# Kernel tuning notes

Measured on AMD Instinct MI355X. Metric: run time of the kernel, lower is better.

The kernel has to match this reference:

```python
import jax, jax.numpy as jnp
import numpy as np

SIGMA = 8.0
C_SIZE = 512
STRIDE = 8
BG_RATIO = 0.15
EPS = 1e-5


def setup_inputs() -> dict:
    key = jax.random.key(0)
    k1, k2 = jax.random.split(key)
    B, N = 16, 512
    # head-point coordinates uniformly in the crop [0, C_SIZE)
    points = jax.random.uniform(k1, (B, N, 2), dtype=jnp.float32) * C_SIZE
    # per-image shortest side sizes, realistic crop scales
    st_sizes = jax.random.uniform(k2, (B,), dtype=jnp.float32) * 256.0 + 256.0
    return {"points": points, "st_sizes": st_sizes}


def reference(points, st_sizes):
    # pixel-center coordinates of the downsampled density grid, [C]
    cood = jnp.arange(0, C_SIZE, STRIDE, dtype=jnp.float32) + STRIDE / 2.0
    B, N, _ = points.shape
    C = cood.shape[0]
    x = points[..., 0]  # [B, N]
    y = points[..., 1]  # [B, N]
    # (x - c)^2 == -2*x*c + x^2 + c^2 (the matmul trick in the original)
    x_dis = (x[..., None] - cood) ** 2  # [B, N, C]
    y_dis = (y[..., None] - cood) ** 2  # [B, N, C]
    # dis[b, p, i, j] = (y_p - cood_i)^2 + (x_p - cood_j)^2
    dis = y_dis[:, :, :, None] + x_dis[:, :, None, :]  # [B, N, C, C]
    dis = dis.reshape(B, N, C * C)  # [B, N, M]
    # background distance: per-pixel min over points, clamped at 0
    min_dis = jnp.clip(jnp.min(dis, axis=1, keepdims=True), 0.0)  # [B, 1, M]
    bg_dis = (st_sizes[:, None, None] * BG_RATIO) ** 2 / (min_dis + EPS)
    dis = jnp.concatenate([dis, bg_dis], axis=1)  # [B, N+1, M]
    logits = -dis / (2.0 * SIGMA ** 2)
    # softmax over the point (+background) axis, per pixel
    return jax.nn.softmax(logits, axis=1)
```

## Files before the change

### kernel.cpp

```cpp
#include <hip/hip_runtime.h>
#include <hip/hip_bf16.h>
#include <cstddef>

constexpr int NPT = 512;
constexpr int C   = 64;
constexpr int M   = C * C;
constexpr int NP1 = NPT + 1;
constexpr float K = 1.0f / 128.0f;
constexpr float BG_RATIO = 0.15f;
constexpr float EPS = 1e-5f;

__global__ __launch_bounds__(256) void pp_kernel(
    const float* __restrict__ points,
    const float* __restrict__ st,
    float* __restrict__ out)
{
    const int b    = blockIdx.x >> 6;
    const int i    = blockIdx.x & 63;
    const int t    = threadIdx.x;
    const int lane = t & 63;
    const int w    = t >> 6;
    const int jg   = t & 15;
    const int pc   = t >> 4;

    const float cy  = (float)(i * 8 + 4);
    const float cx0 = (float)(jg * 32 + 4);
    const float cx1 = cx0 + 8.0f;
    const float cx2 = cx0 + 16.0f;
    const float cx3 = cx0 + 24.0f;

    __shared__ float2 pts[NPT];
    __shared__ float4 redmin[4][16];
    __shared__ float4 redsum[4][16];
    __shared__ float  rs[C];
    __shared__ float  bgs[C];

    const float2* pb = (const float2*)(points + (size_t)b * NPT * 2);
    for (int p = t; p < NPT; p += 256) pts[p] = pb[p];
    __syncthreads();

    const int p0 = pc * 32;

    float4 mn = make_float4(3.4e38f, 3.4e38f, 3.4e38f, 3.4e38f);
    float4 sm = make_float4(0.f, 0.f, 0.f, 0.f);
    #pragma unroll 4
    for (int k = 0; k < 32; ++k) {
        float2 xy = pts[p0 + k];
        float dy  = xy.y - cy;
        float dy2 = dy * dy;
        float dx0 = xy.x - cx0, dx1 = xy.x - cx1, dx2 = xy.x - cx2, dx3 = xy.x - cx3;
        float d0 = fmaf(dx0, dx0, dy2);
        float d1 = fmaf(dx1, dx1, dy2);
        float d2 = fmaf(dx2, dx2, dy2);
        float d3 = fmaf(dx3, dx3, dy2);
        mn.x = fminf(mn.x, d0); mn.y = fminf(mn.y, d1);
        mn.z = fminf(mn.z, d2); mn.w = fminf(mn.w, d3);
        sm.x += __expf(-d0 * K); sm.y += __expf(-d1 * K);
        sm.z += __expf(-d2 * K); sm.w += __expf(-d3 * K);
    }

    #pragma unroll
    for (int off = 16; off <= 32; off <<= 1) {
        mn.x = fminf(mn.x, __shfl_xor(mn.x, off));
        mn.y = fminf(mn.y, __shfl_xor(mn.y, off));
        mn.z = fminf(mn.z, __shfl_xor(mn.z, off));
        mn.w = fminf(mn.w, __shfl_xor(mn.w, off));
        sm.x += __shfl_xor(sm.x, off);
        sm.y += __shfl_xor(sm.y, off);
        sm.z += __shfl_xor(sm.z, off);
        sm.w += __shfl_xor(sm.w, off);
    }
    if (lane < 16) { redmin[w][lane] = mn; redsum[w][lane] = sm; }
    __syncthreads();

    if (t < C) {
        const float* rm = (const float*)redmin;
        const float* rq = (const float*)redsum;
        float m0 = fminf(fminf(rm[t], rm[64 + t]), fminf(rm[128 + t], rm[192 + t]));
        float s0 = (rq[t] + rq[64 + t]) + (rq[128 + t] + rq[192 + t]);
        float ss = st[b] * BG_RATIO;
        float bg = (ss * ss) / (m0 + EPS);
        float tot = s0 + __expf(-bg * K);
        bgs[t] = bg;
        rs[t]  = 1.0f / tot;
    }
    __syncthreads();

    const float4 r4 = *(const float4*)&rs[jg * 4];

    float* ob = out + (size_t)b * NP1 * M + (size_t)p0 * M + i * C + jg * 4;
    #pragma unroll 4
    for (int k = 0; k < 32; ++k) {
        float2 xy = pts[p0 + k];
        float dy  = xy.y - cy;
        float dy2 = dy * dy;
        float dx0 = xy.x - cx0, dx1 = xy.x - cx1, dx2 = xy.x - cx2, dx3 = xy.x - cx3;
        float4 v;
        v.x = __expf(-fmaf(dx0, dx0, dy2) * K) * r4.x;
        v.y = __expf(-fmaf(dx1, dx1, dy2) * K) * r4.y;
        v.z = __expf(-fmaf(dx2, dx2, dy2) * K) * r4.z;
        v.w = __expf(-fmaf(dx3, dx3, dy2) * K) * r4.w;
        *(float4*)(ob + (size_t)k * M) = v;
    }

    if (t < C) {
        out[(size_t)b * NP1 * M + (size_t)NPT * M + i * C + t] =
            __expf(-bgs[t] * K) * rs[t];
    }
}

extern "C" void kernel_launch(void* const* d_in, const int* in_sizes, int n_in,
                              void* d_out, int out_size, void* d_ws, size_t ws_size,
                              hipStream_t stream) {
    const float* points = (const float*)d_in[0];
    const float* st     = (const float*)d_in[1];
    float* out          = (float*)d_out;

    const int B = in_sizes[1];
    dim3 grid(B * C);
    dim3 block(256);
    pp_kernel<<<grid, block, 0, stream>>>(points, st, out);
}
```

Before: 141.1 us.

## Split into denominator and row-contiguous store kernels via workspace

The fused kernel is split in two. The first kernel computes the per-pixel softmax reciprocal and the background channel, and writes the reciprocal to workspace. The second kernel launches one block per (batch, point) and writes each full output row of M floats contiguously, instead of scattered 256-byte chunks across many rows. The exponentials also switch to exp2f with a prescaled constant. The trade-off is an extra launch, a workspace round trip, and recomputing the point loads in the second kernel.

```diff
diff --git a/kernel.cpp b/kernel.cpp
--- a/kernel.cpp
+++ b/kernel.cpp
@@ -6,14 +6,15 @@
 constexpr int C   = 64;
 constexpr int M   = C * C;
 constexpr int NP1 = NPT + 1;
-constexpr float K = 1.0f / 128.0f;
 constexpr float BG_RATIO = 0.15f;
 constexpr float EPS = 1e-5f;
+constexpr float CEXP = -0.011271055f;
 
-__global__ __launch_bounds__(256) void pp_kernel(
+__global__ __launch_bounds__(256) void pp_denom(
     const float* __restrict__ points,
     const float* __restrict__ st,
-    float* __restrict__ out)
+    float* __restrict__ out,
+    float* __restrict__ rsws)
 {
     const int b    = blockIdx.x >> 6;
     const int i    = blockIdx.x & 63;
@@ -32,8 +33,6 @@
     __shared__ float2 pts[NPT];
     __shared__ float4 redmin[4][16];
     __shared__ float4 redsum[4][16];
-    __shared__ float  rs[C];
-    __shared__ float  bgs[C];
 
     const float2* pb = (const float2*)(points + (size_t)b * NPT * 2);
     for (int p = t; p < NPT; p += 256) pts[p] = pb[p];
@@ -55,8 +54,8 @@
         float d3 = fmaf(dx3, dx3, dy2);
         mn.x = fminf(mn.x, d0); mn.y = fminf(mn.y, d1);
         mn.z = fminf(mn.z, d2); mn.w = fminf(mn.w, d3);
-        sm.x += __expf(-d0 * K); sm.y += __expf(-d1 * K);
-        sm.z += __expf(-d2 * K); sm.w += __expf(-d3 * K);
+        sm.x += exp2f(d0 * CEXP); sm.y += exp2f(d1 * CEXP);
+        sm.z += exp2f(d2 * CEXP); sm.w += exp2f(d3 * CEXP);
     }
 
     #pragma unroll
@@ -80,32 +79,42 @@
         float s0 = (rq[t] + rq[64 + t]) + (rq[128 + t] + rq[192 + t]);
         float ss = st[b] * BG_RATIO;
         float bg = (ss * ss) / (m0 + EPS);
-        float tot = s0 + __expf(-bg * K);
-        bgs[t] = bg;
-        rs[t]  = 1.0f / tot;
+        float eb = exp2f(bg * CEXP);
+        float r  = 1.0f / (s0 + eb);
+        rsws[(size_t)b * M + i * C + t] = r;
+        out[(size_t)b * NP1 * M + (size_t)NPT * M + i * C + t] = eb * r;
     }
-    __syncthreads();
+}
 
-    const float4 r4 = *(const float4*)&rs[jg * 4];
+__global__ __launch_bounds__(256) void pp_store(
+    const float* __restrict__ points,
+    const float* __restrict__ rsws,
+    float* __restrict__ out)
+{
+    const int b = blockIdx.x >> 9;
+    const int p = blockIdx.x & 511;
+    const int t = threadIdx.x;
 
-    float* ob = out + (size_t)b * NP1 * M + (size_t)p0 * M + i * C + jg * 4;
-    #pragma unroll 4
-    for (int k = 0; k < 32; ++k) {
-        float2 xy = pts[p0 + k];
-        float dy  = xy.y - cy;
+    const float2 xy = ((const float2*)points)[b * NPT + p];
+    const float* rrow = rsws + (size_t)b * M;
+    float* orow = out + ((size_t)b * NP1 + p) * M;
+
+    #pragma unroll
+    for (int g = 0; g < 4; ++g) {
+        const int m = g * 1024 + t * 4;
+        const int i = m >> 6;
+        const int j = m & 63;
+        float dy  = xy.y - (float)(i * 8 + 4);
         float dy2 = dy * dy;
-        float dx0 = xy.x - cx0, dx1 = xy.x - cx1, dx2 = xy.x - cx2, dx3 = xy.x - cx3;
+        float4 r4 = *(const float4*)(rrow + m);
+        float dx0 = xy.x - (float)(j * 8 + 4);
+        float dx1 = dx0 - 8.0f, dx2 = dx0 - 16.0f, dx3 = dx0 - 24.0f;
         float4 v;
-        v.x = __expf(-fmaf(dx0, dx0, dy2) * K) * r4.x;
-        v.y = __expf(-fmaf(dx1, dx1, dy2) * K) * r4.y;
-        v.z = __expf(-fmaf(dx2, dx2, dy2) * K) * r4.z;
-        v.w = __expf(-fmaf(dx3, dx3, dy2) * K) * r4.w;
-        *(float4*)(ob + (size_t)k * M) = v;
-    }
-
-    if (t < C) {
-        out[(size_t)b * NP1 * M + (size_t)NPT * M + i * C + t] =
-            __expf(-bgs[t] * K) * rs[t];
+        v.x = exp2f(fmaf(dx0, dx0, dy2) * CEXP) * r4.x;
+        v.y = exp2f(fmaf(dx1, dx1, dy2) * CEXP) * r4.y;
+        v.z = exp2f(fmaf(dx2, dx2, dy2) * CEXP) * r4.z;
+        v.w = exp2f(fmaf(dx3, dx3, dy2) * CEXP) * r4.w;
+        *(float4*)(orow + m) = v;
     }
 }
 
@@ -115,9 +124,9 @@
     const float* points = (const float*)d_in[0];
     const float* st     = (const float*)d_in[1];
     float* out          = (float*)d_out;
+    float* rsws         = (float*)d_ws;
 
     const int B = in_sizes[1];
-    dim3 grid(B * C);
-    dim3 block(256);
-    pp_kernel<<<grid, block, 0, stream>>>(points, st, out);
+    pp_denom<<<dim3(B * C), dim3(256), 0, stream>>>(points, st, out, rsws);
+    pp_store<<<dim3(B * NPT), dim3(256), 0, stream>>>(points, rsws, out);
 }
```

After: 146.7 us. +4.0%, slower.
